# Kernel tuning notes

Hardware: AMD Instinct MI355X
Metric: run time of the kernel (lower is better)

## Reference

```python
import jax, jax.numpy as jnp
import numpy as np

HEADS = 4

def _layernorm(x, g, b, eps=1e-5):
    mu = x.mean(-1, keepdims=True)
    var = ((x - mu) ** 2).mean(-1, keepdims=True)
    return (x - mu) / jnp.sqrt(var + eps) * g + b

def _feature_map(data, proj, is_query, eps=1e-4):
    # FAVOR+ softmax kernel features. data: [B,H,S,dh], proj: [m,dh]
    dh = data.shape[-1]
    m = proj.shape[0]
    dn = dh ** -0.25
    ratio = m ** -0.5
    dash = jnp.einsum('bhsd,md->bhsm', data * dn, proj)
    diag = 0.5 * jnp.sum((data * dn) ** 2, axis=-1, keepdims=True)
    mx = jnp.max(dash, axis=-1, keepdims=True) if is_query else jnp.max(dash)
    return ratio * (jnp.exp(dash - diag - mx) + eps)

def _causal_linear_attention(q, k, v):
    # q,k: [B,H,S,m] kernel features; v: [B,H,S,dh]
    k_cum = jnp.cumsum(k, axis=2)                                  # [B,H,S,m]
    d_inv = 1.0 / jnp.einsum('bhsm,bhsm->bhs', q, k_cum)           # [B,H,S]
    ctx = jnp.cumsum(jnp.einsum('bhsm,bhsd->bhsmd', k, v), axis=2) # [B,H,S,m,dh]
    return jnp.einsum('bhsmd,bhsm,bhs->bhsd', ctx, q, d_inv)

def reference(x, pre_w, pre_b, ln1_g, ln1_b, wq, wk, wv, wo, bo, proj,
              ln2_g, ln2_b, ff_w1, ff_b1, ff_w2, ff_b2, tgt_w, tgt_b, rd_w, rd_b):
    # preproc: 1x1x1 conv3d + softplus
    xbn = jax.nn.softplus(jnp.einsum('bcthw,oc->bothw', x, pre_w)
                          + pre_b[None, :, None, None, None])
    B, D, T, H, W = xbn.shape
    tokens = xbn.reshape(B, -1, D)  # raw torch-style reshape, S = T*H*W
    S = tokens.shape[1]

    # Performer block (depth=1): prenorm attention + prenorm FF, residuals
    h = _layernorm(tokens, ln1_g, ln1_b)
    split = lambda t: t.reshape(B, S, HEADS, -1).transpose(0, 2, 1, 3)
    q, k, v = split(h @ wq), split(h @ wk), split(h @ wv)
    qp = _feature_map(q, proj, True)
    kp = _feature_map(k, proj, False)
    attn = _causal_linear_attention(qp, kp, v)
    attn = attn.transpose(0, 2, 1, 3).reshape(B, S, D)
    tokens = tokens + attn @ wo + bo
    h2 = _layernorm(tokens, ln2_g, ln2_b)
    tokens = tokens + jax.nn.gelu(h2 @ ff_w1 + ff_b1, approximate=False) @ ff_w2 + ff_b2

    # readout
    out = tokens.reshape(B, D, T, H, W).mean(axis=2)               # [B,D,H,W]
    out = jnp.concatenate([out, x[:, 2, 0][:, None]], axis=1)      # [B,D+1,H,W]
    out = jax.lax.conv_general_dilated(out, tgt_w, (1, 1), [(2, 2), (2, 2)],
                                       dimension_numbers=('NCHW', 'OIHW', 'NCHW'))
    out = out + tgt_b[None, :, None, None]
    out = out.mean(axis=(2, 3))                                    # global avg pool -> [B,1]
    return out @ rd_w.T + rd_b


def setup_inputs() -> dict:
    key = jax.random.key(0)
    ks = jax.random.split(key, 12)
    B, T, H, W = 2, 8, 48, 48
    D, DH, M, FF = 64, 16, 32, 256
    s = lambda k, shape, sc=1.0: jax.random.normal(k, shape, jnp.float32) * sc
    inv = 1.0 / np.sqrt(D)
    return {
        'x': s(ks[0], (B, 3, T, H, W)),
        'pre_w': s(ks[1], (D, 3), 1.0 / np.sqrt(3)),
        'pre_b': jnp.zeros((D,), jnp.float32),
        'ln1_g': jnp.ones((D,), jnp.float32), 'ln1_b': jnp.zeros((D,), jnp.float32),
        'wq': s(ks[2], (D, D), inv), 'wk': s(ks[3], (D, D), inv), 'wv': s(ks[4], (D, D), inv),
        'wo': s(ks[5], (D, D), inv), 'bo': jnp.zeros((D,), jnp.float32),
        'proj': s(ks[6], (M, DH)),
        'ln2_g': jnp.ones((D,), jnp.float32), 'ln2_b': jnp.zeros((D,), jnp.float32),
        'ff_w1': s(ks[7], (D, FF), inv), 'ff_b1': jnp.zeros((FF,), jnp.float32),
        'ff_w2': s(ks[8], (FF, D), 1.0 / np.sqrt(FF)), 'ff_b2': jnp.zeros((D,), jnp.float32),
        'tgt_w': s(ks[9], (1, D + 1, 5, 5), 1.0 / np.sqrt((D + 1) * 25)),
        'tgt_b': jnp.zeros((1,), jnp.float32),
        'rd_w': s(ks[10], (1, 1)), 'rd_b': jnp.zeros((1,), jnp.float32),
    }
```

## Files before the change

### kernel.cpp

```cpp
#include <hip/hip_runtime.h>
#include <hip/hip_bf16.h>
#include <math.h>

typedef __hip_bfloat16 bf16;
typedef __attribute__((ext_vector_type(8))) short short8;
typedef __attribute__((ext_vector_type(16))) float floatx16;

constexpr int B_   = 2;
constexpr int T_   = 8;
constexpr int HW   = 48 * 48;
constexpr int S_   = T_ * HW;
constexpr int D_   = 64;
constexpr int NH   = 4;
constexpr int DH   = 16;
constexpr int M_   = 32;
constexpr int BS   = B_ * S_;
constexpr int BSD  = BS * D_;
constexpr int BH   = B_ * NH;
constexpr int BHS  = BH * S_;
constexpr int CHUNK = 32;
constexpr int NC   = S_ / CHUNK;
constexpr int NSEG = 18;
constexpr int SEGLEN = 32;
constexpr int STATE = M_ * DH + M_;
constexpr int GSLOTS = 64;
constexpr int GSTRIDE = 32;
constexpr float DN = 0.5f;
constexpr float RATIO = 0.17677669529663687f;

__device__ __forceinline__ unsigned short f2bf(float f) {
  bf16 h = __float2bfloat16(f);
  return *reinterpret_cast<unsigned short*>(&h);
}
__device__ __forceinline__ float bf2f(bf16 v) { return __bfloat162float(v); }
__device__ __forceinline__ float bfs2f(short s) {
  return __uint_as_float(((unsigned)(unsigned short)s) << 16);
}
__device__ __forceinline__ void atomicMaxFloat(float* addr, float val) {
  if (val >= 0.f) atomicMax((int*)addr, __float_as_int(val));
  else atomicMin((unsigned int*)addr, __float_as_uint(val));
}

__global__ void __launch_bounds__(256) k_preqkv(const float* __restrict__ x,
                      const float* __restrict__ pw, const float* __restrict__ pb,
                      const float* __restrict__ g, const float* __restrict__ bb,
                      const float* __restrict__ wq, const float* __restrict__ wk,
                      const float* __restrict__ wv,
                      bf16* __restrict__ tok, bf16* __restrict__ q,
                      bf16* __restrict__ k, bf16* __restrict__ v,
                      float* __restrict__ gmax) {
  __shared__ __align__(16) short sh[32 * 64];
  int tid = threadIdx.x;
  int tbase = blockIdx.x * 32;
  if (blockIdx.x == 0 && tid < GSLOTS)
    ((unsigned*)gmax)[tid * GSTRIDE] = 0xff800000u;

  {
    size_t f0 = (size_t)tbase * 64;
    int b = (int)(f0 / ((size_t)D_ * S_));
    int rem = (int)(f0 % ((size_t)D_ * S_));
    int d = rem / S_;
    int pos0 = rem % S_;
    float w0 = pw[d * 3 + 0], w1 = pw[d * 3 + 1], w2 = pw[d * 3 + 2], pbd = pb[d];
    const float* xb = x + ((size_t)b * 3) * S_ + pos0 + tid * 8;
    float4 x0a = *(const float4*)(xb);
    float4 x0b = *(const float4*)(xb + 4);
    float4 x1a = *(const float4*)(xb + S_);
    float4 x1b = *(const float4*)(xb + S_ + 4);
    float4 x2a = *(const float4*)(xb + 2 * S_);
    float4 x2b = *(const float4*)(xb + 2 * S_ + 4);
    float xf0[8] = {x0a.x, x0a.y, x0a.z, x0a.w, x0b.x, x0b.y, x0b.z, x0b.w};
    float xf1[8] = {x1a.x, x1a.y, x1a.z, x1a.w, x1b.x, x1b.y, x1b.z, x1b.w};
    float xf2[8] = {x2a.x, x2a.y, x2a.z, x2a.w, x2b.x, x2b.y, x2b.z, x2b.w};
    float t[8];
    short8 tv;
#pragma unroll
    for (int j = 0; j < 8; ++j) {
      float a = xf0[j] * w0 + xf1[j] * w1 + xf2[j] * w2 + pbd;
      t[j] = fmaxf(a, 0.f) + log1pf(expf(-fabsf(a)));
      tv[j] = (short)f2bf(t[j]);
    }
    *(short8*)(tok + f0 + (size_t)tid * 8) = tv;
    float s1 = 0.f, s2 = 0.f;
#pragma unroll
    for (int j = 0; j < 8; ++j) { s1 += t[j]; s2 += t[j] * t[j]; }
#pragma unroll
    for (int off = 4; off; off >>= 1) {
      s1 += __shfl_xor(s1, off, 8);
      s2 += __shfl_xor(s2, off, 8);
    }
    float mu = s1 * (1.f / 64.f);
    float var = s2 * (1.f / 64.f) - mu * mu;
    float rs = rsqrtf(var + 1e-5f);
    int tt = tid >> 3, j8 = tid & 7;
    short8 hv;
#pragma unroll
    for (int j = 0; j < 8; ++j) {
      int c = j8 * 8 + j;
      hv[j] = (short)f2bf((t[j] - mu) * rs * g[c] + bb[c]);
    }
    *(short8*)&sh[tt * 64 + ((j8 ^ (tt & 7)) * 8)] = hv;
  }
  __syncthreads();

  int w = tid >> 6;
  if (w < 3) {
    int L = tid & 63;
    int half = L >> 5;
    int n = L & 31;
    const float* wm = (w == 0) ? wq : (w == 1) ? wk : wv;
    bf16* outm = (w == 0) ? q : (w == 1) ? k : v;

    short8 a[4];
#pragma unroll
    for (int c = 0; c < 4; ++c)
      a[c] = *(const short8*)&sh[n * 64 + (((c * 2 + half) ^ (n & 7)) * 8)];
#pragma unroll
    for (int ct = 0; ct < 2; ++ct) {
      int col = ct * 32 + n;
      short8 bfrag[4];
#pragma unroll
      for (int c = 0; c < 4; ++c) {
#pragma unroll
        for (int j = 0; j < 8; ++j)
          bfrag[c][j] = (short)f2bf(wm[(c * 16 + half * 8 + j) * 64 + col]);
      }
      floatx16 acc;
#pragma unroll
      for (int i = 0; i < 16; ++i) acc[i] = 0.f;
      acc = __builtin_amdgcn_mfma_f32_32x32x16_bf16(a[0], bfrag[0], acc, 0, 0, 0);
      acc = __builtin_amdgcn_mfma_f32_32x32x16_bf16(a[1], bfrag[1], acc, 0, 0, 0);
      acc = __builtin_amdgcn_mfma_f32_32x32x16_bf16(a[2], bfrag[2], acc, 0, 0, 0);
      acc = __builtin_amdgcn_mfma_f32_32x32x16_bf16(a[3], bfrag[3], acc, 0, 0, 0);
      int head = col >> 4, di = col & 15;
#pragma unroll
      for (int r = 0; r < 16; ++r) {
        int row = (r & 3) + 8 * (r >> 2) + 4 * half;
        int token = tbase + row;
        int b = token / S_, s = token % S_;
        outm[((size_t)(b * NH + head) * S_ + s) * DH + di] = __float2bfloat16(acc[r]);
      }
    }
  }
}

__global__ void __launch_bounds__(256) k_feat(const bf16* __restrict__ q,
                      const bf16* __restrict__ k, const float* __restrict__ proj,
                      bf16* __restrict__ qpb, float* __restrict__ gmax) {
  int tid = threadIdx.x;
  int w = tid >> 6;
  int L = tid & 63;
  int half = L >> 5;
  int n = L & 31;
  int rowbase = blockIdx.x * 128 + w * 32;

  short8 qs = *(const short8*)(q + (size_t)(rowbase + n) * 16 + half * 8);
  short8 ks = *(const short8*)(k + (size_t)(rowbase + n) * 16 + half * 8);
  short8 aq, ak, bp;
  float dq = 0.f;
#pragma unroll
  for (int j = 0; j < 8; ++j) {
    float qf = bfs2f(qs[j]) * DN;
    float kf = bfs2f(ks[j]) * DN;
    dq += qf * qf;
    aq[j] = (short)f2bf(qf);
    ak[j] = (short)f2bf(kf);
    bp[j] = (short)f2bf(proj[n * 16 + half * 8 + j]);
  }
  dq += __shfl_xor(dq, 32);
  dq *= 0.5f;

  floatx16 Pq, Pk;
#pragma unroll
  for (int i = 0; i < 16; ++i) { Pq[i] = 0.f; Pk[i] = 0.f; }
  Pq = __builtin_amdgcn_mfma_f32_32x32x16_bf16(aq, bp, Pq, 0, 0, 0);
  Pk = __builtin_amdgcn_mfma_f32_32x32x16_bf16(ak, bp, Pk, 0, 0, 0);

  float bmax = -3.4e38f;
#pragma unroll
  for (int r = 0; r < 16; ++r) bmax = fmaxf(bmax, Pk[r]);

#pragma unroll
  for (int r = 0; r < 16; ++r) {
    int i = (r & 3) + 8 * (r >> 2) + 4 * half;
    float mx = Pq[r];
    for (int off = 16; off; off >>= 1) mx = fmaxf(mx, __shfl_xor(mx, off, 32));
    float dqi = __shfl(dq, i, 64);
    float val = RATIO * (expf(Pq[r] - dqi - mx) + 1e-4f);
    qpb[(size_t)(rowbase + i) * 32 + n] = __float2bfloat16(val);
  }
  for (int off = 32; off; off >>= 1) bmax = fmaxf(bmax, __shfl_xor(bmax, off));
  if (L == 0)
    atomicMaxFloat(&gmax[((blockIdx.x * 4 + w) & (GSLOTS - 1)) * GSTRIDE], bmax);
}

__global__ void __launch_bounds__(256) k_csfin(const float* __restrict__ gmax,
                      const bf16* __restrict__ v, const bf16* __restrict__ k,
                      const float* __restrict__ proj,
                      bf16* __restrict__ kpb, float* __restrict__ ckv) {
  __shared__ __align__(16) float sKp[CHUNK * 32];
  __shared__ __align__(16) float sVc[CHUNK * 16];
  int blk = blockIdx.x;
  int bh = blk / NC, c = blk % NC;
  int tid = threadIdx.x;
  int base = bh * S_ + c * CHUNK;
  int w = tid >> 6, L = tid & 63, half = L >> 5, n = L & 31;
  if (w == 0) {
    float gm = gmax[L * GSTRIDE];
    for (int off = 32; off; off >>= 1) gm = fmaxf(gm, __shfl_xor(gm, off));
    short8 ks = *(const short8*)(k + (size_t)(base + n) * 16 + half * 8);
    short8 ak, bp;
    float dk = 0.f;
#pragma unroll
    for (int j = 0; j < 8; ++j) {
      float kf = bfs2f(ks[j]) * DN;
      dk += kf * kf;
      ak[j] = (short)f2bf(kf);
      bp[j] = (short)f2bf(proj[n * 16 + half * 8 + j]);
    }
    dk += __shfl_xor(dk, 32);
    dk *= 0.5f;
    floatx16 Pk;
#pragma unroll
    for (int i = 0; i < 16; ++i) Pk[i] = 0.f;
    Pk = __builtin_amdgcn_mfma_f32_32x32x16_bf16(ak, bp, Pk, 0, 0, 0);
#pragma unroll
    for (int r = 0; r < 16; ++r) {
      int i = (r & 3) + 8 * (r >> 2) + 4 * half;
      float dgi = __shfl(dk, i, 64);
      sKp[i * 32 + n] = RATIO * (expf(Pk[r] - dgi - gm) + 1e-4f);
    }
  } else if (w == 1) {
    int row = L >> 1, h8 = (L & 1) * 8;
    short8 vs = *(const short8*)(v + (size_t)(base + row) * 16 + h8);
#pragma unroll
    for (int j = 0; j < 8; ++j) sVc[row * 16 + h8 + j] = bfs2f(vs[j]);
  }
  __syncthreads();
  {
    int row = tid >> 3, m4 = tid & 7;
    float4 fin = *(const float4*)&sKp[row * 32 + m4 * 4];
    uint2 u;
    u.x = (unsigned)f2bf(fin.x) | ((unsigned)f2bf(fin.y) << 16);
    u.y = (unsigned)f2bf(fin.z) | ((unsigned)f2bf(fin.w) << 16);
    *(uint2*)&kpb[(size_t)(base + row) * 32 + m4 * 4] = u;
  }
  int m0 = tid >> 4, d0 = tid & 15;
  int m1 = m0 + 16;
  float a0 = 0.f, a1 = 0.f, az0 = 0.f, az1 = 0.f;
  for (int t = 0; t < CHUNK; ++t) {
    float k0 = sKp[t * 32 + m0];
    float k1 = sKp[t * 32 + m1];
    float vv = sVc[t * 16 + d0];
    a0 += k0 * vv;
    a1 += k1 * vv;
    if (d0 == 0) { az0 += k0; az1 += k1; }
  }
  float* outp = ckv + (size_t)blk * STATE;
  outp[m0 * 16 + d0] = a0;
  outp[m1 * 16 + d0] = a1;
  if (d0 == 0) { outp[512 + m0] = az0; outp[512 + m1] = az1; }
}

__global__ void k_scan1(const float* __restrict__ ckv, float* __restrict__ segsum) {
  int idx = blockIdx.x * 256 + threadIdx.x;
  int c = idx % STATE;
  int rem = idx / STATE;
  int seg = rem % NSEG;
  int bh = rem / NSEG;
  size_t base = ((size_t)bh * NC + seg * SEGLEN) * STATE + c;
  float s = 0.f;
#pragma unroll 8
  for (int i = 0; i < SEGLEN; ++i) s += ckv[base + (size_t)i * STATE];
  segsum[idx] = s;
}

__global__ void k_scan23(float* __restrict__ ckv, const float* __restrict__ segsum) {
  int idx = blockIdx.x * 256 + threadIdx.x;
  int c = idx % STATE;
  int rem = idx / STATE;
  int seg = rem % NSEG;
  int bh = rem / NSEG;
  const float* sb = segsum + (size_t)bh * NSEG * STATE + c;
  float run = 0.f;
  for (int s = 0; s < seg; ++s) run += sb[(size_t)s * STATE];
  size_t base = ((size_t)bh * NC + seg * SEGLEN) * STATE + c;
  for (int i0 = 0; i0 < SEGLEN; i0 += 8) {
    float tb[8];
#pragma unroll
    for (int j = 0; j < 8; ++j) tb[j] = ckv[base + (size_t)(i0 + j) * STATE];
#pragma unroll
    for (int j = 0; j < 8; ++j) {
      ckv[base + (size_t)(i0 + j) * STATE] = run;
      run += tb[j];
    }
  }
}

__global__ void __launch_bounds__(256) k_attn(const bf16* __restrict__ qpb,
                                              const bf16* __restrict__ kpb,
                                              const bf16* __restrict__ v,
                                              const float* __restrict__ ckv,
                                              bf16* __restrict__ attn) {
  __shared__ __align__(16) float sP[4][32 * 33 + 4];
  int tid = threadIdx.x;
  int w = tid >> 6;
  int L = tid & 63;
  int half = L >> 5;
  int n = L & 31;
  int chunk = blockIdx.x * 4 + w;
  int bh = chunk / NC, c = chunk % NC;
  int base = bh * S_ + c * CHUNK;

  short8 a1 = *(const short8*)(qpb + (size_t)(base + n) * 32 + half * 8);
  short8 a2 = *(const short8*)(qpb + (size_t)(base + n) * 32 + 16 + half * 8);
  short8 b1 = *(const short8*)(kpb + (size_t)(base + n) * 32 + half * 8);
  short8 b2 = *(const short8*)(kpb + (size_t)(base + n) * 32 + 16 + half * 8);

  floatx16 P;
#pragma unroll
  for (int i = 0; i < 16; ++i) P[i] = 0.f;
  P = __builtin_amdgcn_mfma_f32_32x32x16_bf16(a1, b1, P, 0, 0, 0);
  P = __builtin_amdgcn_mfma_f32_32x32x16_bf16(a2, b2, P, 0, 0, 0);

  float* sp = &sP[w][0];
#pragma unroll
  for (int r = 0; r < 16; ++r) {
    int i = (r & 3) + 8 * (r >> 2) + 4 * half;
    sp[i * 33 + n] = (n <= i) ? P[r] : 0.f;
  }
  __syncthreads();
  short8 pa1, pa2;
#pragma unroll
  for (int j = 0; j < 8; ++j) {
    pa1[j] = (short)f2bf(sp[n * 33 + half * 8 + j]);
    pa2[j] = (short)f2bf(sp[n * 33 + 16 + half * 8 + j]);
  }

  const float* cs = ckv + (size_t)chunk * STATE;
  const unsigned short one_bf = f2bf(1.f);
  short8 vb1, vb2, sb1, sb2;
#pragma unroll
  for (int j = 0; j < 8; ++j) {
    int t1 = half * 8 + j, t2 = 16 + half * 8 + j;
    vb1[j] = (n < 16) ? *(const short*)(v + (size_t)(base + t1) * 16 + n)
                      : (short)(n == 16 ? one_bf : 0);
    vb2[j] = (n < 16) ? *(const short*)(v + (size_t)(base + t2) * 16 + n)
                      : (short)(n == 16 ? one_bf : 0);
    float y1 = (n < 16) ? cs[t1 * 16 + n] : (n == 16 ? cs[512 + t1] : 0.f);
    float y2 = (n < 16) ? cs[t2 * 16 + n] : (n == 16 ? cs[512 + t2] : 0.f);
    sb1[j] = (short)f2bf(y1);
    sb2[j] = (short)f2bf(y2);
  }

  floatx16 O;
#pragma unroll
  for (int i = 0; i < 16; ++i) O[i] = 0.f;
  O = __builtin_amdgcn_mfma_f32_32x32x16_bf16(pa1, vb1, O, 0, 0, 0);
  O = __builtin_amdgcn_mfma_f32_32x32x16_bf16(pa2, vb2, O, 0, 0, 0);
  O = __builtin_amdgcn_mfma_f32_32x32x16_bf16(a1, sb1, O, 0, 0, 0);
  O = __builtin_amdgcn_mfma_f32_32x32x16_bf16(a2, sb2, O, 0, 0, 0);

  int srcl = 16 + 32 * half;
  float res[16];
#pragma unroll
  for (int r = 0; r < 16; ++r) {
    float den = __shfl(O[r], srcl, 64);
    res[r] = O[r] / den;
  }
  if (n < 16) {
    int b = bh >> 2, head = bh & 3;
#pragma unroll
    for (int r = 0; r < 16; ++r) {
      int i = (r & 3) + 8 * (r >> 2) + 4 * half;
      attn[((size_t)(b * S_ + c * CHUNK + i)) * 64 + head * 16 + n] = __float2bfloat16(res[r]);
// ... 42 lines not shown
    sC[row * 68 + col] = acc[r] + bf2f(tok[(size_t)(tbase + row) * 64 + col]) + bias;
  }
  __syncthreads();
  int tg = tid >> 5, cg = tid & 31;
  int c0 = cg * 2, c1 = c0 + 1;
  float g0 = g[c0], g1 = g[c1], be0 = bb[c0], be1 = bb[c1];
#pragma unroll
  for (int i = 0; i < 8; ++i) {
    int lrow = tg * 8 + i;
    int token = tbase + lrow;
    float t0 = sC[lrow * 68 + c0];
    float t1 = sC[lrow * 68 + c1];
    float s1 = t0 + t1, s2 = t0 * t0 + t1 * t1;
    for (int off = 16; off; off >>= 1) {
      s1 += __shfl_xor(s1, off, 32);
      s2 += __shfl_xor(s2, off, 32);
    }
    float mu = s1 * (1.f / 64.f);
    float var = s2 * (1.f / 64.f) - mu * mu;
    float rs = rsqrtf(var + 1e-5f);
    tok2[token * 64 + c0] = __float2bfloat16(t0);
    tok2[token * 64 + c1] = __float2bfloat16(t1);
    h2[token * 64 + c0] = __float2bfloat16((t0 - mu) * rs * g0 + be0);
    h2[token * 64 + c1] = __float2bfloat16((t1 - mu) * rs * g1 + be1);
  }
}

__global__ void __launch_bounds__(256) k_ffg(const bf16* __restrict__ h2,
                                             const float* __restrict__ w1,
                                             const float* __restrict__ b1,
                                             float* __restrict__ Gavg) {
  int tid = threadIdx.x;
  int w = tid >> 6;
  int L = tid & 63;
  int half = L >> 5;
  int n = L & 31;
  int blk = blockIdx.x;
  int b = blk / 576;
  int rem = blk % 576;
  int ch = rem / 9;
  int jp0 = (rem % 9) * 4;
  int token_n = b * 18432 + ch * 288 + (n & 7) * 36 + jp0 + (n >> 3);

  short8 a[4];
  {
    const bf16* hrow = h2 + (size_t)token_n * 64 + half * 8;
#pragma unroll
    for (int c = 0; c < 4; ++c) a[c] = *(const short8*)(hrow + c * 16);
  }
  size_t gbase = ((size_t)(b * 64 + ch) * 36 + jp0);
#pragma unroll
  for (int ct = 0; ct < 2; ++ct) {
    int col = w * 64 + ct * 32 + n;
    short8 bfrag[4];
#pragma unroll
    for (int c = 0; c < 4; ++c) {
#pragma unroll
      for (int j = 0; j < 8; ++j)
        bfrag[c][j] = (short)f2bf(w1[(c * 16 + half * 8 + j) * 256 + col]);
    }
    floatx16 acc;
#pragma unroll
    for (int i = 0; i < 16; ++i) acc[i] = 0.f;
    acc = __builtin_amdgcn_mfma_f32_32x32x16_bf16(a[0], bfrag[0], acc, 0, 0, 0);
    acc = __builtin_amdgcn_mfma_f32_32x32x16_bf16(a[1], bfrag[1], acc, 0, 0, 0);
    acc = __builtin_amdgcn_mfma_f32_32x32x16_bf16(a[2], bfrag[2], acc, 0, 0, 0);
    acc = __builtin_amdgcn_mfma_f32_32x32x16_bf16(a[3], bfrag[3], acc, 0, 0, 0);
    float bias = b1[col];
#pragma unroll
    for (int j = 0; j < 4; ++j) {
      float s = 0.f;
#pragma unroll
      for (int rr = 0; rr < 4; ++rr) {
        float xg = acc[j * 4 + rr] + bias;
        s += 0.5f * xg * (1.f + erff(xg * 0.70710678118654752f));
      }
      s += __shfl_xor(s, 32);
      if (half == 0)
        Gavg[(gbase + j) * 256 + col] = s * 0.125f;
    }
  }
}

__global__ void __launch_bounds__(256) k_pool2(const float* __restrict__ Gavg,
                        const bf16* __restrict__ tok2, const float* __restrict__ w2,
                        const float* __restrict__ b2, float* __restrict__ pool) {
  __shared__ __align__(16) float sG[18 * 256];
  __shared__ __align__(16) float sRed[4 * 18 * 64];
  int blk = blockIdx.x;
  int b = blk / 128;
  int rem = blk % 128;
  int ch = rem >> 1, jph = rem & 1;
  int tid = threadIdx.x;
  size_t grow0 = ((size_t)(b * 64 + ch) * 36 + jph * 18) * 256;
  for (int e = tid; e < 1152; e += 256) {
    int row = e >> 6, c4 = e & 63;
    *(float4*)&sG[row * 256 + c4 * 4] = *(const float4*)&Gavg[grow0 + row * 256 + c4 * 4];
  }
  __syncthreads();
  int kg = tid >> 6, dd = tid & 63;
  float acc[18];
#pragma unroll
  for (int i = 0; i < 18; ++i) acc[i] = 0.f;
  for (int k4 = 0; k4 < 16; ++k4) {
    int k = kg * 64 + k4 * 4;
    float w0 = w2[(k + 0) * 64 + dd];
    float w1 = w2[(k + 1) * 64 + dd];
    float w2v = w2[(k + 2) * 64 + dd];
    float w3 = w2[(k + 3) * 64 + dd];
#pragma unroll
    for (int i = 0; i < 18; ++i) {
      float4 gf = *(const float4*)&sG[i * 256 + k];
      acc[i] += gf.x * w0 + gf.y * w1 + gf.z * w2v + gf.w * w3;
    }
  }
#pragma unroll
  for (int i = 0; i < 18; ++i) sRed[(kg * 18 + i) * 64 + dd] = acc[i];
  __syncthreads();
  for (int o = tid; o < 1152; o += 256) {
    int jp18 = o >> 6, d2 = o & 63;
    float gsum = sRed[(0 * 18 + jp18) * 64 + d2] + sRed[(1 * 18 + jp18) * 64 + d2]
               + sRed[(2 * 18 + jp18) * 64 + d2] + sRed[(3 * 18 + jp18) * 64 + d2];
    int p = (jph * 18 + jp18) * 64 + d2;
    size_t tbase = (size_t)b * 1179648 + (size_t)ch * 18432 + p;
    float ts = 0.f;
#pragma unroll
    for (int t = 0; t < 8; ++t) ts += bf2f(tok2[tbase + t * 2304]);
    pool[((size_t)(b * 64 + ch)) * HW + p] = ts * 0.125f + gsum + b2[d2];
  }
}

__global__ void __launch_bounds__(256) k_convsum(const float* __restrict__ pool,
                                                 const float* __restrict__ x,
                                                 const float* __restrict__ w,
                                                 float* __restrict__ partial) {
  int blk = blockIdx.x;
  int b = blk / 65, ch = blk % 65;
  int tid = threadIdx.x;
  __shared__ float cls[25];
  __shared__ float red[256];
  if (tid < 25) {
    int ry = tid / 5, rx = tid % 5;
    int kh0 = (ry <= 2) ? 0 : (ry == 3 ? 1 : 2);
    int kh1 = (ry >= 2) ? 4 : (ry == 1 ? 3 : 2);
    int kw0 = (rx <= 2) ? 0 : (rx == 3 ? 1 : 2);
    int kw1 = (rx >= 2) ? 4 : (rx == 1 ? 3 : 2);
    float s = 0.f;
    for (int kh = kh0; kh <= kh1; ++kh)
      for (int kw = kw0; kw <= kw1; ++kw)
        s += w[ch * 25 + kh * 5 + kw];
    cls[tid] = s;
  }
  __syncthreads();
  const float* pc = (ch < 64) ? (pool + ((size_t)(b * 64 + ch)) * HW)
                              : (x + (size_t)b * 3 * S_ + 2 * S_);
  float acc = 0.f;
#pragma unroll
  for (int e = tid; e < HW; e += 256) {
    int iy = e / 48, ix = e % 48;
    int ry = (iy == 0) ? 0 : (iy == 1) ? 1 : (iy <= 45) ? 2 : (iy == 46) ? 3 : 4;
    int rx = (ix == 0) ? 0 : (ix == 1) ? 1 : (ix <= 45) ? 2 : (ix == 46) ? 3 : 4;
    acc += pc[e] * cls[ry * 5 + rx];
  }
  red[tid] = acc;
  __syncthreads();
  for (int s = 128; s; s >>= 1) {
    if (tid < s) red[tid] += red[tid + s];
    __syncthreads();
  }
  if (!tid) partial[blk] = red[0];
}

__global__ void k_final(const float* __restrict__ partial, const float* __restrict__ tgt_b,
                        const float* __restrict__ rd_w, const float* __restrict__ rd_b,
                        float* __restrict__ out) {
  int b = blockIdx.x;
  int lane = threadIdx.x;
  float s = (lane < 65) ? partial[b * 65 + lane] : 0.f;
  for (int off = 32; off; off >>= 1) s += __shfl_down(s, off, 64);
  __shared__ float r2;
  if (lane == 64) r2 = s;
  __syncthreads();
  if (!lane) {
    float tot = s + r2;
    float mean = tot / 2304.f + tgt_b[0];
    out[b] = mean * rd_w[0] + rd_b[0];
  }
}

extern "C" void kernel_launch(void* const* d_in, const int* in_sizes, int n_in,
                              void* d_out, int out_size, void* d_ws, size_t ws_size,
                              hipStream_t stream) {
  const float* x     = (const float*)d_in[0];
  const float* pre_w = (const float*)d_in[1];
  const float* pre_b = (const float*)d_in[2];
  const float* ln1_g = (const float*)d_in[3];
  const float* ln1_b = (const float*)d_in[4];
  const float* wq    = (const float*)d_in[5];
  const float* wk    = (const float*)d_in[6];
  const float* wv    = (const float*)d_in[7];
  const float* wo    = (const float*)d_in[8];
  const float* bo    = (const float*)d_in[9];
  const float* proj  = (const float*)d_in[10];
  const float* ln2_g = (const float*)d_in[11];
  const float* ln2_b = (const float*)d_in[12];
  const float* ff_w1 = (const float*)d_in[13];
  const float* ff_b1 = (const float*)d_in[14];
  const float* ff_w2 = (const float*)d_in[15];
  const float* ff_b2 = (const float*)d_in[16];
  const float* tgt_w = (const float*)d_in[17];
  const float* tgt_b = (const float*)d_in[18];
  const float* rd_w  = (const float*)d_in[19];
  const float* rd_b  = (const float*)d_in[20];
  float* out = (float*)d_out;

  float* ws = (float*)d_ws;
  bf16*  tok   = (bf16*)ws;
  bf16*  v     = (bf16*)(ws + (size_t)BSD);
  bf16*  q     = (bf16*)(ws + 2 * (size_t)BSD);
  float* Gavg  = ws + 2 * (size_t)BSD;
  float* pool  = Gavg + 1179648;
  bf16*  k     = (bf16*)(ws + 3 * (size_t)BSD);
  bf16*  h2    = (bf16*)(ws + 4 * (size_t)BSD);
  bf16*  qpb   = (bf16*)(ws + 6 * (size_t)BSD);
  bf16*  kpb   = (bf16*)(ws + 7 * (size_t)BSD);
  float* ckv   = ws + 8 * (size_t)BSD;
  bf16*  tok2  = (bf16*)(ws + 8 * (size_t)BSD);
  bf16*  attnb = k;
  float* smalls = ws + 9 * (size_t)BSD + 147456;
  float* gmax  = smalls;
  float* partial = smalls + 2048;
  float* segsum  = smalls + 2304;

  k_preqkv<<<dim3(BS / 32), dim3(256), 0, stream>>>(x, pre_w, pre_b, ln1_g, ln1_b,
                                                    wq, wk, wv, tok, q, k, v, gmax);
  k_feat<<<dim3(BHS / 128), dim3(256), 0, stream>>>(q, k, proj, qpb, gmax);
  k_csfin<<<dim3(BH * NC), dim3(256), 0, stream>>>(gmax, v, k, proj, kpb, ckv);
  k_scan1<<<dim3(BH * NSEG * STATE / 256), dim3(256), 0, stream>>>(ckv, segsum);
  k_scan23<<<dim3(BH * NSEG * STATE / 256), dim3(256), 0, stream>>>(ckv, segsum);
  k_attn<<<dim3(BH * NC / 4), dim3(256), 0, stream>>>(qpb, kpb, v, ckv, attnb);
  k_wo_ln<<<dim3(BS / 32), dim3(128), 0, stream>>>(attnb, wo, bo, tok, ln2_g, ln2_b, tok2, h2);
  k_ffg<<<dim3(B_ * 64 * 9), dim3(256), 0, stream>>>(h2, ff_w1, ff_b1, Gavg);
  k_pool2<<<dim3(B_ * 64 * 2), dim3(256), 0, stream>>>(Gavg, tok2, ff_w2, ff_b2, pool);
  k_convsum<<<dim3(B_ * 65), dim3(256), 0, stream>>>(pool, x, tgt_w, partial);
  k_final<<<dim3(B_), dim3(128), 0, stream>>>(partial, tgt_b, rd_w, rd_b, out);
}
```

Baseline: 206.7 us.

## Fuse feature map into QKV kernel, merge scan passes, fuse pool with conv

Computes the query FAVOR+ features and the key block max inside the QKV projection kernel, keeping q and k in shared memory so q is never written to global memory. The two-pass segmented cumulative scan becomes one kernel that reduces run sums in shared memory. The pooling/FF2 stage is fused with the border-class convolution reduction, and the extra channel folds into the final kernel. This cuts launches and global round trips, but fewer blocks in poolconv (128) and scan may lower parallelism.

```diff
diff --git a/kernel.cpp b/kernel.cpp
--- a/kernel.cpp
+++ b/kernel.cpp
@@ -20,11 +20,12 @@
 constexpr int BHS  = BH * S_;
 constexpr int CHUNK = 32;
 constexpr int NC   = S_ / CHUNK;
-constexpr int NSEG = 18;
-constexpr int SEGLEN = 32;
 constexpr int STATE = M_ * DH + M_;
 constexpr int GSLOTS = 64;
 constexpr int GSTRIDE = 32;
+constexpr int SCB = 16;
+constexpr int SRG = 16;
+constexpr int SRUN = NC / SRG;
 constexpr float DN = 0.5f;
 constexpr float RATIO = 0.17677669529663687f;
 
@@ -45,15 +46,14 @@
                       const float* __restrict__ pw, const float* __restrict__ pb,
                       const float* __restrict__ g, const float* __restrict__ bb,
                       const float* __restrict__ wq, const float* __restrict__ wk,
-                      const float* __restrict__ wv,
-                      bf16* __restrict__ tok, bf16* __restrict__ q,
-                      bf16* __restrict__ k, bf16* __restrict__ v,
-                      float* __restrict__ gmax) {
+                      const float* __restrict__ wv, const float* __restrict__ proj,
+                      bf16* __restrict__ tok, bf16* __restrict__ k, bf16* __restrict__ v,
+                      bf16* __restrict__ qpb, float* __restrict__ gmax) {
   __shared__ __align__(16) short sh[32 * 64];
+  __shared__ __align__(16) short sq[32 * 64];
+  __shared__ __align__(16) short sk[32 * 64];
   int tid = threadIdx.x;
   int tbase = blockIdx.x * 32;
-  if (blockIdx.x == 0 && tid < GSLOTS)
-    ((unsigned*)gmax)[tid * GSTRIDE] = 0xff800000u;
 
   {
     size_t f0 = (size_t)tbase * 64;
@@ -104,13 +104,12 @@
   __syncthreads();
 
   int w = tid >> 6;
+  int L = tid & 63;
+  int half = L >> 5;
+  int n = L & 31;
+
   if (w < 3) {
-    int L = tid & 63;
-    int half = L >> 5;
-    int n = L & 31;
     const float* wm = (w == 0) ? wq : (w == 1) ? wk : wv;
-    bf16* outm = (w == 0) ? q : (w == 1) ? k : v;
-
     short8 a[4];
 #pragma unroll
     for (int c = 0; c < 4; ++c)
@@ -136,62 +135,67 @@
 #pragma unroll
       for (int r = 0; r < 16; ++r) {
         int row = (r & 3) + 8 * (r >> 2) + 4 * half;
-        int token = tbase + row;
-        int b = token / S_, s = token % S_;
-        outm[((size_t)(b * NH + head) * S_ + s) * DH + di] = __float2bfloat16(acc[r]);
+        if (w == 2) {
+          int token = tbase + row;
+          int b = token / S_, s = token % S_;
+          v[((size_t)(b * NH + head) * S_ + s) * DH + di] = __float2bfloat16(acc[r]);
+        } else {
+          unsigned short us = f2bf(acc[r]);
+          if (w == 1) {
+            int token = tbase + row;
+            int b = token / S_, s = token % S_;
+            k[((size_t)(b * NH + head) * S_ + s) * DH + di] = *(bf16*)&us;
+          }
+          float scv = bfs2f((short)us) * DN;
+          unsigned short usv = f2bf(scv);
+          short* dst = (w == 0) ? sq : sk;
+          *(short*)((char*)dst + row * 128 + ((col * 2) ^ ((row & 7) << 4))) = (short)usv;
+        }
       }
     }
   }
-}
-
-__global__ void __launch_bounds__(256) k_feat(const bf16* __restrict__ q,
-                      const bf16* __restrict__ k, const float* __restrict__ proj,
-                      bf16* __restrict__ qpb, float* __restrict__ gmax) {
-  int tid = threadIdx.x;
-  int w = tid >> 6;
-  int L = tid & 63;
-  int half = L >> 5;
-  int n = L & 31;
-  int rowbase = blockIdx.x * 128 + w * 32;
-
-  short8 qs = *(const short8*)(q + (size_t)(rowbase + n) * 16 + half * 8);
-  short8 ks = *(const short8*)(k + (size_t)(rowbase + n) * 16 + half * 8);
-  short8 aq, ak, bp;
-  float dq = 0.f;
-#pragma unroll
-  for (int j = 0; j < 8; ++j) {
-    float qf = bfs2f(qs[j]) * DN;
-    float kf = bfs2f(ks[j]) * DN;
-    dq += qf * qf;
-    aq[j] = (short)f2bf(qf);
-    ak[j] = (short)f2bf(kf);
-    bp[j] = (short)f2bf(proj[n * 16 + half * 8 + j]);
-  }
-  dq += __shfl_xor(dq, 32);
-  dq *= 0.5f;
-
-  floatx16 Pq, Pk;
-#pragma unroll
-  for (int i = 0; i < 16; ++i) { Pq[i] = 0.f; Pk[i] = 0.f; }
-  Pq = __builtin_amdgcn_mfma_f32_32x32x16_bf16(aq, bp, Pq, 0, 0, 0);
-  Pk = __builtin_amdgcn_mfma_f32_32x32x16_bf16(ak, bp, Pk, 0, 0, 0);
-
-  float bmax = -3.4e38f;
-#pragma unroll
-  for (int r = 0; r < 16; ++r) bmax = fmaxf(bmax, Pk[r]);
-
-#pragma unroll
-  for (int r = 0; r < 16; ++r) {
-    int i = (r & 3) + 8 * (r >> 2) + 4 * half;
-    float mx = Pq[r];
-    for (int off = 16; off; off >>= 1) mx = fmaxf(mx, __shfl_xor(mx, off, 32));
-    float dqi = __shfl(dq, i, 64);
-    float val = RATIO * (expf(Pq[r] - dqi - mx) + 1e-4f);
-    qpb[(size_t)(rowbase + i) * 32 + n] = __float2bfloat16(val);
-  }
-  for (int off = 32; off; off >>= 1) bmax = fmaxf(bmax, __shfl_xor(bmax, off));
-  if (L == 0)
-    atomicMaxFloat(&gmax[((blockIdx.x * 4 + w) & (GSLOTS - 1)) * GSTRIDE], bmax);
+  __syncthreads();
+
+  {
+    int h = w;
+    short8 bp, aq, ak;
+#pragma unroll
+    for (int j = 0; j < 8; ++j)
+      bp[j] = (short)f2bf(proj[n * 16 + half * 8 + j]);
+    int roff = n * 128 + ((h * 32 + half * 16) ^ ((n & 7) << 4));
+    aq = *(const short8*)((const char*)sq + roff);
+    ak = *(const short8*)((const char*)sk + roff);
+    float dq = 0.f;
+#pragma unroll
+    for (int j = 0; j < 8; ++j) { float f = bfs2f(aq[j]); dq += f * f; }
+    dq += __shfl_xor(dq, 32);
+    dq *= 0.5f;
+
+    floatx16 Pq, Pk;
+#pragma unroll
+    for (int i = 0; i < 16; ++i) { Pq[i] = 0.f; Pk[i] = 0.f; }
+    Pq = __builtin_amdgcn_mfma_f32_32x32x16_bf16(aq, bp, Pq, 0, 0, 0);
+    Pk = __builtin_amdgcn_mfma_f32_32x32x16_bf16(ak, bp, Pk, 0, 0, 0);
+
+    float bmax = -3.4e38f;
+#pragma unroll
+    for (int r = 0; r < 16; ++r) bmax = fmaxf(bmax, Pk[r]);
+
+#pragma unroll
+    for (int r = 0; r < 16; ++r) {
+      int i = (r & 3) + 8 * (r >> 2) + 4 * half;
+      float mx = Pq[r];
+      for (int off = 16; off; off >>= 1) mx = fmaxf(mx, __shfl_xor(mx, off, 32));
+      float dqi = __shfl(dq, i, 64);
+      float val = RATIO * (expf(Pq[r] - dqi - mx) + 1e-4f);
+      int token = tbase + i;
+      int b = token / S_, s = token % S_;
+      qpb[((size_t)(b * NH + h) * S_ + s) * 32 + n] = __float2bfloat16(val);
+    }
+    for (int off = 32; off; off >>= 1) bmax = fmaxf(bmax, __shfl_xor(bmax, off));
+    if (L == 0)
+      atomicMaxFloat(&gmax[((blockIdx.x * 4 + h) & (GSLOTS - 1)) * GSTRIDE], bmax);
+  }
 }
 
 __global__ void __launch_bounds__(256) k_csfin(const float* __restrict__ gmax,
@@ -262,35 +266,28 @@
   if (d0 == 0) { outp[512 + m0] = az0; outp[512 + m1] = az1; }
 }
 
-__global__ void k_scan1(const float* __restrict__ ckv, float* __restrict__ segsum) {
-  int idx = blockIdx.x * 256 + threadIdx.x;
-  int c = idx % STATE;
-  int rem = idx / STATE;
-  int seg = rem % NSEG;
-  int bh = rem / NSEG;
-  size_t base = ((size_t)bh * NC + seg * SEGLEN) * STATE + c;
+__global__ void __launch_bounds__(256) k_scan(float* __restrict__ ckv) {
+  __shared__ float sS[SRG][SCB];
+  int blk = blockIdx.x;
+  int bh = blk / (STATE / SCB);
+  int c0 = (blk % (STATE / SCB)) * SCB;
+  int cl = threadIdx.x & (SCB - 1);
+  int rg = threadIdx.x >> 4;
+  int c = c0 + cl;
+  size_t base = ((size_t)bh * NC + rg * SRUN) * STATE + c;
   float s = 0.f;
-#pragma unroll 8
-  for (int i = 0; i < SEGLEN; ++i) s += ckv[base + (size_t)i * STATE];
-  segsum[idx] = s;
-}
-
-__global__ void k_scan23(float* __restrict__ ckv, const float* __restrict__ segsum) {
-  int idx = blockIdx.x * 256 + threadIdx.x;
-  int c = idx % STATE;
-  int rem = idx / STATE;
-  int seg = rem % NSEG;
-  int bh = rem / NSEG;
-  const float* sb = segsum + (size_t)bh * NSEG * STATE + c;
+#pragma unroll 6
+  for (int i = 0; i < SRUN; ++i) s += ckv[base + (size_t)i * STATE];
+  sS[rg][cl] = s;
+  __syncthreads();
   float run = 0.f;
-  for (int s = 0; s < seg; ++s) run += sb[(size_t)s * STATE];
-  size_t base = ((size_t)bh * NC + seg * SEGLEN) * STATE + c;
-  for (int i0 = 0; i0 < SEGLEN; i0 += 8) {
-    float tb[8];
-#pragma unroll
-    for (int j = 0; j < 8; ++j) tb[j] = ckv[base + (size_t)(i0 + j) * STATE];
-#pragma unroll
-    for (int j = 0; j < 8; ++j) {
+  for (int r = 0; r < rg; ++r) run += sS[r][cl];
+  for (int i0 = 0; i0 < SRUN; i0 += 6) {
+    float tb[6];
+#pragma unroll
+    for (int j = 0; j < 6; ++j) tb[j] = ckv[base + (size_t)(i0 + j) * STATE];
+#pragma unroll
+    for (int j = 0; j < 6; ++j) {
       ckv[base + (size_t)(i0 + j) * STATE] = run;
       run += tb[j];
     }
@@ -499,60 +496,92 @@
   }
 }
 
-__global__ void __launch_bounds__(256) k_pool2(const float* __restrict__ Gavg,
+__global__ void __launch_bounds__(256) k_poolconv(const float* __restrict__ Gavg,
                         const bf16* __restrict__ tok2, const float* __restrict__ w2,
-                        const float* __restrict__ b2, float* __restrict__ pool) {
+                        const float* __restrict__ b2, const float* __restrict__ w,
+                        float* __restrict__ partial) {
   __shared__ __align__(16) float sG[18 * 256];
   __shared__ __align__(16) float sRed[4 * 18 * 64];
+  __shared__ __align__(16) float sPool[HW];
+  __shared__ float cls[25];
+  __shared__ float red[256];
   int blk = blockIdx.x;
-  int b = blk / 128;
-  int rem = blk % 128;
-  int ch = rem >> 1, jph = rem & 1;
+  int b = blk >> 6, ch = blk & 63;
   int tid = threadIdx.x;
-  size_t grow0 = ((size_t)(b * 64 + ch) * 36 + jph * 18) * 256;
-  for (int e = tid; e < 1152; e += 256) {
-    int row = e >> 6, c4 = e & 63;
-    *(float4*)&sG[row * 256 + c4 * 4] = *(const float4*)&Gavg[grow0 + row * 256 + c4 * 4];
-  }
-  __syncthreads();
-  int kg = tid >> 6, dd = tid & 63;
-  float acc[18];
-#pragma unroll
-  for (int i = 0; i < 18; ++i) acc[i] = 0.f;
-  for (int k4 = 0; k4 < 16; ++k4) {
-    int k = kg * 64 + k4 * 4;
-    float w0 = w2[(k + 0) * 64 + dd];
-    float w1 = w2[(k + 1) * 64 + dd];
-    float w2v = w2[(k + 2) * 64 + dd];
-    float w3 = w2[(k + 3) * 64 + dd];
-#pragma unroll
-    for (int i = 0; i < 18; ++i) {
-      float4 gf = *(const float4*)&sG[i * 256 + k];
-      acc[i] += gf.x * w0 + gf.y * w1 + gf.z * w2v + gf.w * w3;
-    }
-  }
-#pragma unroll
-  for (int i = 0; i < 18; ++i) sRed[(kg * 18 + i) * 64 + dd] = acc[i];
-  __syncthreads();
-  for (int o = tid; o < 1152; o += 256) {
-    int jp18 = o >> 6, d2 = o & 63;
-    float gsum = sRed[(0 * 18 + jp18) * 64 + d2] + sRed[(1 * 18 + jp18) * 64 + d2]
-               + sRed[(2 * 18 + jp18) * 64 + d2] + sRed[(3 * 18 + jp18) * 64 + d2];
-    int p = (jph * 18 + jp18) * 64 + d2;
-    size_t tbase = (size_t)b * 1179648 + (size_t)ch * 18432 + p;
-    float ts = 0.f;
-#pragma unroll
-    for (int t = 0; t < 8; ++t) ts += bf2f(tok2[tbase + t * 2304]);
-    pool[((size_t)(b * 64 + ch)) * HW + p] = ts * 0.125f + gsum + b2[d2];
-  }
-}
-
-__global__ void __launch_bounds__(256) k_convsum(const float* __restrict__ pool,
-                                                 const float* __restrict__ x,
-                                                 const float* __restrict__ w,
-                                                 float* __restrict__ partial) {
-  int blk = blockIdx.x;
-  int b = blk / 65, ch = blk % 65;
+  if (tid < 25) {
+    int ry = tid / 5, rx = tid % 5;
+    int kh0 = (ry <= 2) ? 0 : (ry == 3 ? 1 : 2);
+    int kh1 = (ry >= 2) ? 4 : (ry == 1 ? 3 : 2);
+    int kw0 = (rx <= 2) ? 0 : (rx == 3 ? 1 : 2);
+    int kw1 = (rx >= 2) ? 4 : (rx == 1 ? 3 : 2);
+    float s = 0.f;
+    for (int kh = kh0; kh <= kh1; ++kh)
+      for (int kw = kw0; kw <= kw1; ++kw)
+        s += w[ch * 25 + kh * 5 + kw];
+    cls[tid] = s;
+  }
+  for (int jph = 0; jph < 2; ++jph) {
+    size_t grow0 = ((size_t)(b * 64 + ch) * 36 + jph * 18) * 256;
+    for (int e = tid; e < 1152; e += 256) {
+      int row = e >> 6, c4 = e & 63;
+      *(float4*)&sG[row * 256 + c4 * 4] = *(const float4*)&Gavg[grow0 + row * 256 + c4 * 4];
+    }
+    __syncthreads();
+    int kg = tid >> 6, dd = tid & 63;
+    float acc[18];
+#pragma unroll
+    for (int i = 0; i < 18; ++i) acc[i] = 0.f;
+    for (int k4 = 0; k4 < 16; ++k4) {
+      int kk = kg * 64 + k4 * 4;
+      float w0 = w2[(kk + 0) * 64 + dd];
+      float w1 = w2[(kk + 1) * 64 + dd];
+      float w2v = w2[(kk + 2) * 64 + dd];
+      float w3 = w2[(kk + 3) * 64 + dd];
+#pragma unroll
+      for (int i = 0; i < 18; ++i) {
+        float4 gf = *(const float4*)&sG[i * 256 + kk];
+        acc[i] += gf.x * w0 + gf.y * w1 + gf.z * w2v + gf.w * w3;
+      }
+    }
+#pragma unroll
+    for (int i = 0; i < 18; ++i) sRed[(kg * 18 + i) * 64 + dd] = acc[i];
+    __syncthreads();
+    for (int o = tid; o < 1152; o += 256) {
+      int jp18 = o >> 6, d2 = o & 63;
+      float gsum = sRed[(0 * 18 + jp18) * 64 + d2] + sRed[(1 * 18 + jp18) * 64 + d2]
+                 + sRed[(2 * 18 + jp18) * 64 + d2] + sRed[(3 * 18 + jp18) * 64 + d2];
+      int p = (jph * 18 + jp18) * 64 + d2;
+      size_t tbase = (size_t)b * 1179648 + (size_t)ch * 18432 + p;
+      float ts = 0.f;
+#pragma unroll
+      for (int t = 0; t < 8; ++t) ts += bf2f(tok2[tbase + t * 2304]);
+      sPool[p] = ts * 0.125f + gsum + b2[d2];
+    }
+    __syncthreads();
+  }
+  float acc = 0.f;
+#pragma unroll
+  for (int e = tid; e < HW; e += 256) {
+    int iy = e / 48, ix = e % 48;
+    int ry = (iy == 0) ? 0 : (iy == 1) ? 1 : (iy <= 45) ? 2 : (iy == 46) ? 3 : 4;
+    int rx = (ix == 0) ? 0 : (ix == 1) ? 1 : (ix <= 45) ? 2 : (ix == 46) ? 3 : 4;
+    acc += sPool[e] * cls[ry * 5 + rx];
+  }
+  red[tid] = acc;
+  __syncthreads();
+  for (int s = 128; s; s >>= 1) {
+    if (tid < s) red[tid] += red[tid + s];
+    __syncthreads();
+  }
+  if (!tid) partial[blk] = red[0];
+}
+
+__global__ void __launch_bounds__(256) k_final(const float* __restrict__ partial,
+                        const float* __restrict__ x, const float* __restrict__ w,
+                        const float* __restrict__ tgt_b,
+                        const float* __restrict__ rd_w, const float* __restrict__ rd_b,
+                        float* __restrict__ out) {
+  int b = blockIdx.x;
   int tid = threadIdx.x;
   __shared__ float cls[25];
   __shared__ float red[256];
@@ -565,12 +594,11 @@
     float s = 0.f;
     for (int kh = kh0; kh <= kh1; ++kh)
       for (int kw = kw0; kw <= kw1; ++kw)
-        s += w[ch * 25 + kh * 5 + kw];
+        s += w[64 * 25 + kh * 5 + kw];
     cls[tid] = s;
   }
   __syncthreads();
-  const float* pc = (ch < 64) ? (pool + ((size_t)(b * 64 + ch)) * HW)
-                              : (x + (size_t)b * 3 * S_ + 2 * S_);
+  const float* pc = x + (size_t)b * 3 * S_ + 2 * S_;
   float acc = 0.f;
 #pragma unroll
   for (int e = tid; e < HW; e += 256) {
@@ -579,28 +607,15 @@
     int rx = (ix == 0) ? 0 : (ix == 1) ? 1 : (ix <= 45) ? 2 : (ix == 46) ? 3 : 4;
     acc += pc[e] * cls[ry * 5 + rx];
   }
+  if (tid < 64) acc += partial[b * 64 + tid];
   red[tid] = acc;
   __syncthreads();
   for (int s = 128; s; s >>= 1) {
     if (tid < s) red[tid] += red[tid + s];
     __syncthreads();
   }
-  if (!tid) partial[blk] = red[0];
-}
-
-__global__ void k_final(const float* __restrict__ partial, const float* __restrict__ tgt_b,
-                        const float* __restrict__ rd_w, const float* __restrict__ rd_b,
-                        float* __restrict__ out) {
-  int b = blockIdx.x;
-  int lane = threadIdx.x;
-  float s = (lane < 65) ? partial[b * 65 + lane] : 0.f;
-  for (int off = 32; off; off >>= 1) s += __shfl_down(s, off, 64);
-  __shared__ float r2;
-  if (lane == 64) r2 = s;
-  __syncthreads();
-  if (!lane) {
-    float tot = s + r2;
-    float mean = tot / 2304.f + tgt_b[0];
+  if (!tid) {
+    float mean = red[0] / 2304.f + tgt_b[0];
     out[b] = mean * rd_w[0] + rd_b[0];
   }
 }
@@ -634,9 +649,7 @@
   float* ws = (float*)d_ws;
   bf16*  tok   = (bf16*)ws;
   bf16*  v     = (bf16*)(ws + (size_t)BSD);
-  bf16*  q     = (bf16*)(ws + 2 * (size_t)BSD);
   float* Gavg  = ws + 2 * (size_t)BSD;
-  float* pool  = Gavg + 1179648;
   bf16*  k     = (bf16*)(ws + 3 * (size_t)BSD);
   bf16*  h2    = (bf16*)(ws + 4 * (size_t)BSD);
   bf16*  qpb   = (bf16*)(ws + 6 * (size_t)BSD);
@@ -647,18 +660,15 @@
   float* smalls = ws + 9 * (size_t)BSD + 147456;
   float* gmax  = smalls;
   float* partial = smalls + 2048;
-  float* segsum  = smalls + 2304;
-
+
+  hipMemsetAsync(gmax, 0xFF, GSLOTS * GSTRIDE * sizeof(float), stream);
   k_preqkv<<<dim3(BS / 32), dim3(256), 0, stream>>>(x, pre_w, pre_b, ln1_g, ln1_b,
-                                                    wq, wk, wv, tok, q, k, v, gmax);
-  k_feat<<<dim3(BHS / 128), dim3(256), 0, stream>>>(q, k, proj, qpb, gmax);
+                                                    wq, wk, wv, proj, tok, k, v, qpb, gmax);
   k_csfin<<<dim3(BH * NC), dim3(256), 0, stream>>>(gmax, v, k, proj, kpb, ckv);
-  k_scan1<<<dim3(BH * NSEG * STATE / 256), dim3(256), 0, stream>>>(ckv, segsum);
-  k_scan23<<<dim3(BH * NSEG * STATE / 256), dim3(256), 0, stream>>>(ckv, segsum);
+  k_scan<<<dim3(BH * (STATE / SCB)), dim3(256), 0, stream>>>(ckv);
   k_attn<<<dim3(BH * NC / 4), dim3(256), 0, stream>>>(qpb, kpb, v, ckv, attnb);
   k_wo_ln<<<dim3(BS / 32), dim3(128), 0, stream>>>(attnb, wo, bo, tok, ln2_g, ln2_b, tok2, h2);
   k_ffg<<<dim3(B_ * 64 * 9), dim3(256), 0, stream>>>(h2, ff_w1, ff_b1, Gavg);
-  k_pool2<<<dim3(B_ * 64 * 2), dim3(256), 0, stream>>>(Gavg, tok2, ff_w2, ff_b2, pool);
-  k_convsum<<<dim3(B_ * 65), dim3(256), 0, stream>>>(pool, x, tgt_w, partial);
-  k_final<<<dim3(B_), dim3(128), 0, stream>>>(partial, tgt_b, rd_w, rd_b, out);
-}
+  k_poolconv<<<dim3(B_ * 64), dim3(256), 0, stream>>>(Gavg, tok2, ff_w2, ff_b2, tgt_w, partial);
+  k_final<<<dim3(B_), dim3(256), 0, stream>>>(partial, x, tgt_w, tgt_b, rd_w, rd_b, out);
+}
```

Result: slower. 217.7 us (+5.3%).

## Fuse key max into QKV kernel, merge feature/chunk kernels, single-pass scan

Applied to the files above, without the earlier changes.

Computes the key feature-map global max inside the QKV projection kernel using a shared-memory copy of scaled K, so the separate feature kernel no longer has to reread K. The query feature computation is merged into the chunk-state kernel as extra blocks in a single launch. The two-kernel segmented scan is replaced by one kernel that reduces and scans within a block through shared memory. The gmax init moves to a memset. The goal is fewer launches and less global traffic, at the cost of a QKV kernel that does more work and uses more shared memory.

```diff
diff --git a/kernel.cpp b/kernel.cpp
--- a/kernel.cpp
+++ b/kernel.cpp
@@ -20,11 +20,12 @@
 constexpr int BHS  = BH * S_;
 constexpr int CHUNK = 32;
 constexpr int NC   = S_ / CHUNK;
-constexpr int NSEG = 18;
-constexpr int SEGLEN = 32;
 constexpr int STATE = M_ * DH + M_;
 constexpr int GSLOTS = 64;
 constexpr int GSTRIDE = 32;
+constexpr int SCB = 16;
+constexpr int SRG = 16;
+constexpr int SRUN = NC / SRG;
 constexpr float DN = 0.5f;
 constexpr float RATIO = 0.17677669529663687f;
 
@@ -45,15 +46,14 @@
                       const float* __restrict__ pw, const float* __restrict__ pb,
                       const float* __restrict__ g, const float* __restrict__ bb,
                       const float* __restrict__ wq, const float* __restrict__ wk,
-                      const float* __restrict__ wv,
+                      const float* __restrict__ wv, const float* __restrict__ proj,
                       bf16* __restrict__ tok, bf16* __restrict__ q,
                       bf16* __restrict__ k, bf16* __restrict__ v,
                       float* __restrict__ gmax) {
   __shared__ __align__(16) short sh[32 * 64];
+  __shared__ __align__(16) short sk[32 * 64];
   int tid = threadIdx.x;
   int tbase = blockIdx.x * 32;
-  if (blockIdx.x == 0 && tid < GSLOTS)
-    ((unsigned*)gmax)[tid * GSTRIDE] = 0xff800000u;
 
   {
     size_t f0 = (size_t)tbase * 64;
@@ -104,10 +104,11 @@
   __syncthreads();
 
   int w = tid >> 6;
+  int L = tid & 63;
+  int half = L >> 5;
+  int n = L & 31;
+
   if (w < 3) {
-    int L = tid & 63;
-    int half = L >> 5;
-    int n = L & 31;
     const float* wm = (w == 0) ? wq : (w == 1) ? wk : wv;
     bf16* outm = (w == 0) ? q : (w == 1) ? k : v;
 
@@ -138,73 +139,82 @@
         int row = (r & 3) + 8 * (r >> 2) + 4 * half;
         int token = tbase + row;
         int b = token / S_, s = token % S_;
-        outm[((size_t)(b * NH + head) * S_ + s) * DH + di] = __float2bfloat16(acc[r]);
+        unsigned short us = f2bf(acc[r]);
+        outm[((size_t)(b * NH + head) * S_ + s) * DH + di] = *(bf16*)&us;
+        if (w == 1) {
+          float scv = bfs2f((short)us) * DN;
+          *(short*)((char*)sk + row * 128 + ((col * 2) ^ ((row & 7) << 4)))
+              = (short)f2bf(scv);
+        }
       }
     }
   }
-}
-
-__global__ void __launch_bounds__(256) k_feat(const bf16* __restrict__ q,
-                      const bf16* __restrict__ k, const float* __restrict__ proj,
-                      bf16* __restrict__ qpb, float* __restrict__ gmax) {
-  int tid = threadIdx.x;
-  int w = tid >> 6;
-  int L = tid & 63;
-  int half = L >> 5;
-  int n = L & 31;
-  int rowbase = blockIdx.x * 128 + w * 32;
-
-  short8 qs = *(const short8*)(q + (size_t)(rowbase + n) * 16 + half * 8);
-  short8 ks = *(const short8*)(k + (size_t)(rowbase + n) * 16 + half * 8);
-  short8 aq, ak, bp;
-  float dq = 0.f;
-#pragma unroll
-  for (int j = 0; j < 8; ++j) {
-    float qf = bfs2f(qs[j]) * DN;
-    float kf = bfs2f(ks[j]) * DN;
-    dq += qf * qf;
-    aq[j] = (short)f2bf(qf);
-    ak[j] = (short)f2bf(kf);
-    bp[j] = (short)f2bf(proj[n * 16 + half * 8 + j]);
-  }
-  dq += __shfl_xor(dq, 32);
-  dq *= 0.5f;
-
-  floatx16 Pq, Pk;
-#pragma unroll
-  for (int i = 0; i < 16; ++i) { Pq[i] = 0.f; Pk[i] = 0.f; }
-  Pq = __builtin_amdgcn_mfma_f32_32x32x16_bf16(aq, bp, Pq, 0, 0, 0);
-  Pk = __builtin_amdgcn_mfma_f32_32x32x16_bf16(ak, bp, Pk, 0, 0, 0);
-
-  float bmax = -3.4e38f;
-#pragma unroll
-  for (int r = 0; r < 16; ++r) bmax = fmaxf(bmax, Pk[r]);
-
-#pragma unroll
-  for (int r = 0; r < 16; ++r) {
-    int i = (r & 3) + 8 * (r >> 2) + 4 * half;
-    float mx = Pq[r];
-    for (int off = 16; off; off >>= 1) mx = fmaxf(mx, __shfl_xor(mx, off, 32));
-    float dqi = __shfl(dq, i, 64);
-    float val = RATIO * (expf(Pq[r] - dqi - mx) + 1e-4f);
-    qpb[(size_t)(rowbase + i) * 32 + n] = __float2bfloat16(val);
-  }
-  for (int off = 32; off; off >>= 1) bmax = fmaxf(bmax, __shfl_xor(bmax, off));
-  if (L == 0)
-    atomicMaxFloat(&gmax[((blockIdx.x * 4 + w) & (GSLOTS - 1)) * GSTRIDE], bmax);
-}
-
-__global__ void __launch_bounds__(256) k_csfin(const float* __restrict__ gmax,
-                      const bf16* __restrict__ v, const bf16* __restrict__ k,
-                      const float* __restrict__ proj,
-                      bf16* __restrict__ kpb, float* __restrict__ ckv) {
+  __syncthreads();
+
+  {
+    short8 bp, ak;
+#pragma unroll
+    for (int j = 0; j < 8; ++j)
+      bp[j] = (short)f2bf(proj[n * 16 + half * 8 + j]);
+    int roff = n * 128 + ((w * 32 + half * 16) ^ ((n & 7) << 4));
+    ak = *(const short8*)((const char*)sk + roff);
+    floatx16 Pk;
+#pragma unroll
+    for (int i = 0; i < 16; ++i) Pk[i] = 0.f;
+    Pk = __builtin_amdgcn_mfma_f32_32x32x16_bf16(ak, bp, Pk, 0, 0, 0);
+    float bmax = -3.4e38f;
+#pragma unroll
+    for (int r = 0; r < 16; ++r) bmax = fmaxf(bmax, Pk[r]);
+    for (int off = 32; off; off >>= 1) bmax = fmaxf(bmax, __shfl_xor(bmax, off));
+    if (L == 0)
+      atomicMaxFloat(&gmax[((blockIdx.x * 4 + w) & (GSLOTS - 1)) * GSTRIDE], bmax);
+  }
+}
+
+__global__ void __launch_bounds__(256) k_featcsfin(const float* __restrict__ gmax,
+                      const bf16* __restrict__ q, const bf16* __restrict__ k,
+                      const bf16* __restrict__ v, const float* __restrict__ proj,
+                      bf16* __restrict__ qpb, bf16* __restrict__ kpb,
+                      float* __restrict__ ckv) {
   __shared__ __align__(16) float sKp[CHUNK * 32];
   __shared__ __align__(16) float sVc[CHUNK * 16];
+  int tid = threadIdx.x;
+  int w = tid >> 6, L = tid & 63, half = L >> 5, n = L & 31;
+
+  if (blockIdx.x >= BH * NC) {
+    int fblk = blockIdx.x - BH * NC;
+    int rowbase = fblk * 128 + w * 32;
+    short8 qs = *(const short8*)(q + (size_t)(rowbase + n) * 16 + half * 8);
+    short8 aq, bp;
+    float dq = 0.f;
+#pragma unroll
+    for (int j = 0; j < 8; ++j) {
+      float qf = bfs2f(qs[j]) * DN;
+      dq += qf * qf;
+      aq[j] = (short)f2bf(qf);
+      bp[j] = (short)f2bf(proj[n * 16 + half * 8 + j]);
+    }
+    dq += __shfl_xor(dq, 32);
+    dq *= 0.5f;
+    floatx16 Pq;
+#pragma unroll
+    for (int i = 0; i < 16; ++i) Pq[i] = 0.f;
+    Pq = __builtin_amdgcn_mfma_f32_32x32x16_bf16(aq, bp, Pq, 0, 0, 0);
+#pragma unroll
+    for (int r = 0; r < 16; ++r) {
+      int i = (r & 3) + 8 * (r >> 2) + 4 * half;
+      float mx = Pq[r];
+      for (int off = 16; off; off >>= 1) mx = fmaxf(mx, __shfl_xor(mx, off, 32));
+      float dqi = __shfl(dq, i, 64);
+      float val = RATIO * (expf(Pq[r] - dqi - mx) + 1e-4f);
+      qpb[(size_t)(rowbase + i) * 32 + n] = __float2bfloat16(val);
+    }
+    return;
+  }
+
   int blk = blockIdx.x;
   int bh = blk / NC, c = blk % NC;
-  int tid = threadIdx.x;
   int base = bh * S_ + c * CHUNK;
-  int w = tid >> 6, L = tid & 63, half = L >> 5, n = L & 31;
   if (w == 0) {
     float gm = gmax[L * GSTRIDE];
     for (int off = 32; off; off >>= 1) gm = fmaxf(gm, __shfl_xor(gm, off));
@@ -262,35 +272,28 @@
   if (d0 == 0) { outp[512 + m0] = az0; outp[512 + m1] = az1; }
 }
 
-__global__ void k_scan1(const float* __restrict__ ckv, float* __restrict__ segsum) {
-  int idx = blockIdx.x * 256 + threadIdx.x;
-  int c = idx % STATE;
-  int rem = idx / STATE;
-  int seg = rem % NSEG;
-  int bh = rem / NSEG;
-  size_t base = ((size_t)bh * NC + seg * SEGLEN) * STATE + c;
+__global__ void __launch_bounds__(256) k_scan(float* __restrict__ ckv) {
+  __shared__ float sS[SRG][SCB];
+  int blk = blockIdx.x;
+  int bh = blk / (STATE / SCB);
+  int c0 = (blk % (STATE / SCB)) * SCB;
+  int cl = threadIdx.x & (SCB - 1);
+  int rg = threadIdx.x >> 4;
+  int c = c0 + cl;
+  size_t base = ((size_t)bh * NC + rg * SRUN) * STATE + c;
   float s = 0.f;
-#pragma unroll 8
-  for (int i = 0; i < SEGLEN; ++i) s += ckv[base + (size_t)i * STATE];
-  segsum[idx] = s;
-}
-
-__global__ void k_scan23(float* __restrict__ ckv, const float* __restrict__ segsum) {
-  int idx = blockIdx.x * 256 + threadIdx.x;
-  int c = idx % STATE;
-  int rem = idx / STATE;
-  int seg = rem % NSEG;
-  int bh = rem / NSEG;
-  const float* sb = segsum + (size_t)bh * NSEG * STATE + c;
+#pragma unroll 6
+  for (int i = 0; i < SRUN; ++i) s += ckv[base + (size_t)i * STATE];
+  sS[rg][cl] = s;
+  __syncthreads();
   float run = 0.f;
-  for (int s = 0; s < seg; ++s) run += sb[(size_t)s * STATE];
-  size_t base = ((size_t)bh * NC + seg * SEGLEN) * STATE + c;
-  for (int i0 = 0; i0 < SEGLEN; i0 += 8) {
-    float tb[8];
-#pragma unroll
-    for (int j = 0; j < 8; ++j) tb[j] = ckv[base + (size_t)(i0 + j) * STATE];
-#pragma unroll
-    for (int j = 0; j < 8; ++j) {
+  for (int r = 0; r < rg; ++r) run += sS[r][cl];
+  for (int i0 = 0; i0 < SRUN; i0 += 6) {
+    float tb[6];
+#pragma unroll
+    for (int j = 0; j < 6; ++j) tb[j] = ckv[base + (size_t)(i0 + j) * STATE];
+#pragma unroll
+    for (int j = 0; j < 6; ++j) {
       ckv[base + (size_t)(i0 + j) * STATE] = run;
       run += tb[j];
     }
@@ -647,14 +650,13 @@
   float* smalls = ws + 9 * (size_t)BSD + 147456;
   float* gmax  = smalls;
   float* partial = smalls + 2048;
-  float* segsum  = smalls + 2304;
-
+
+  hipMemsetAsync(gmax, 0xFF, GSLOTS * GSTRIDE * sizeof(float), stream);
   k_preqkv<<<dim3(BS / 32), dim3(256), 0, stream>>>(x, pre_w, pre_b, ln1_g, ln1_b,
-                                                    wq, wk, wv, tok, q, k, v, gmax);
-  k_feat<<<dim3(BHS / 128), dim3(256), 0, stream>>>(q, k, proj, qpb, gmax);
-  k_csfin<<<dim3(BH * NC), dim3(256), 0, stream>>>(gmax, v, k, proj, kpb, ckv);
-  k_scan1<<<dim3(BH * NSEG * STATE / 256), dim3(256), 0, stream>>>(ckv, segsum);
-  k_scan23<<<dim3(BH * NSEG * STATE / 256), dim3(256), 0, stream>>>(ckv, segsum);
+                                                    wq, wk, wv, proj, tok, q, k, v, gmax);
+  k_featcsfin<<<dim3(BH * NC + BHS / 128), dim3(256), 0, stream>>>(gmax, q, k, v, proj,
+                                                                   qpb, kpb, ckv);
+  k_scan<<<dim3(BH * (STATE / SCB)), dim3(256), 0, stream>>>(ckv);
   k_attn<<<dim3(BH * NC / 4), dim3(256), 0, stream>>>(qpb, kpb, v, ckv, attnb);
   k_wo_ln<<<dim3(BS / 32), dim3(128), 0, stream>>>(attnb, wo, bo, tok, ln2_g, ln2_b, tok2, h2);
   k_ffg<<<dim3(B_ * 64 * 9), dim3(256), 0, stream>>>(h2, ff_w1, ff_b1, Gavg);
```

New measurement: 205.1 us. Within noise of the previous version (-0.7%).
